# Kernel tuning notes

Measured on AMD Instinct MI355X. Metric: run time of the kernel, lower is better.

## Reference

```python
import jax, jax.numpy as jnp
import numpy as np

IN_FEATURES = 4096
OUT_FEATURES = 4096
NNZ = 1677722  # round(0.1 * 4096 * 4096)
N_TOKENS = 8192


def setup_inputs() -> dict:
    key = jax.random.key(0)
    k1, k2, k3, k4 = jax.random.split(key, 4)
    inputs = jax.random.normal(k1, (N_TOKENS, IN_FEATURES), dtype=jnp.float32)
    bound = 1.0 / IN_FEATURES ** 0.5
    weights = jax.random.uniform(k2, (NNZ,), minval=-bound, maxval=bound, dtype=jnp.float32)
    bias = jax.random.uniform(k3, (OUT_FEATURES,), minval=-bound, maxval=bound, dtype=jnp.float32)
    # COO indices: row (output) and col (input) indices, sampled like np.random.choice
    flat = jax.random.randint(k4, (NNZ,), 0, IN_FEATURES * OUT_FEATURES)
    row_ind = flat // IN_FEATURES
    col_ind = flat % IN_FEATURES
    indices = jnp.stack((row_ind, col_ind)).astype(jnp.int64)
    return {"inputs": inputs, "weights": weights, "bias": bias, "indices": indices}


def reference(inputs, weights, bias, indices):
    # Densify COO weight (duplicates are summed, matching torch coalesce/to_dense)
    dense_w = jnp.zeros((OUT_FEATURES, IN_FEATURES), dtype=weights.dtype)
    dense_w = dense_w.at[indices[0], indices[1]].add(weights)
    # output = (W @ x^T)^T + b  ==  x @ W^T + b
    out = jnp.einsum('ni,oi->no', inputs, dense_w) + bias
    return out
```

## Files before the change

### kernel.cpp

```cpp
#include <hip/hip_runtime.h>

#define M_TOK 8192
#define NF    4096
#define KF    4096
#define NHALF 128

typedef __attribute__((ext_vector_type(8))) short bf16x8;
typedef __attribute__((ext_vector_type(4))) float f32x4;
typedef __attribute__((ext_vector_type(2))) short s16x2;

__device__ __forceinline__ unsigned short f2bf(float f) {
    unsigned u = __builtin_bit_cast(unsigned, f);
    u += 0x7FFFu + ((u >> 16) & 1u);
    return (unsigned short)(u >> 16);
}

__device__ __forceinline__ float bf2f(unsigned short b) {
    unsigned u = ((unsigned)b) << 16;
    return __builtin_bit_cast(float, u);
}

__device__ __forceinline__ void load_lds16(const unsigned short* g, unsigned short* l) {
    __builtin_amdgcn_global_load_lds(
        (const __attribute__((address_space(1))) unsigned int*)g,
        (__attribute__((address_space(3))) unsigned int*)l,
        16, 0, 0);
}

__device__ __forceinline__ void block_bar() {
    asm volatile("" ::: "memory");
    __builtin_amdgcn_s_barrier();
    asm volatile("" ::: "memory");
}

#define VMCNT(n) asm volatile("s_waitcnt vmcnt(" #n ")" ::: "memory")

__global__ void prep_zero_convx(const float4* __restrict__ X, ushort4* __restrict__ Xb,
                                uint4* __restrict__ Wb, int nx4, int nwb) {
    int i = blockIdx.x * blockDim.x + threadIdx.x;
    if (i < nwb) Wb[i] = (uint4){0u, 0u, 0u, 0u};
    if (i < nx4) {
        float4 v = X[i];
        ushort4 o;
        o.x = f2bf(v.x); o.y = f2bf(v.y); o.z = f2bf(v.z); o.w = f2bf(v.w);
        Xb[i] = o;
    }
}

__global__ void scatter_bf16(const int* __restrict__ idx, const float* __restrict__ w,
                             unsigned short* __restrict__ Wb, int nnz) {
    int t = blockIdx.x * blockDim.x + threadIdx.x;
    if (t >= nnz) return;
    int r = idx[t];
    int c = idx[nnz + t];
    size_t elem = (size_t)r * KF + c;
#if __has_builtin(__builtin_amdgcn_global_atomic_fadd_v2bf16)
    unsigned short wb = f2bf(w[t]);
    s16x2 val;
    if (elem & 1) { val[0] = 0; val[1] = (short)wb; }
    else          { val[0] = (short)wb; val[1] = 0; }
    __builtin_amdgcn_global_atomic_fadd_v2bf16(
        (__attribute__((address_space(1))) s16x2*)(Wb + (elem & ~(size_t)1)), val);
#else
    unsigned* addr = (unsigned*)(Wb + (elem & ~(size_t)1));
    float wf = w[t];
    unsigned old = __hip_atomic_load(addr, __ATOMIC_RELAXED, __HIP_MEMORY_SCOPE_AGENT), assumed;
    do {
        assumed = old;
        unsigned short cur = (elem & 1) ? (unsigned short)(assumed >> 16)
                                        : (unsigned short)(assumed & 0xffffu);
        unsigned short nw = f2bf(bf2f(cur) + wf);
        unsigned newv = (elem & 1) ? ((assumed & 0x0000ffffu) | ((unsigned)nw << 16))
                                   : ((assumed & 0xffff0000u) | (unsigned)nw);
        old = atomicCAS(addr, assumed, newv);
    } while (old != assumed);
#endif
}

__global__ __launch_bounds__(512, 2) void gemm_bt_bias(
    const unsigned short* __restrict__ A,
    const unsigned short* __restrict__ B,
    const float* __restrict__ bias,
    float* __restrict__ C)
{
    __shared__ unsigned short lds_u[65536];
    char* const ldsb = (char*)lds_u;

    const int tid  = threadIdx.x;
    const int lane = tid & 63;
    const int wave = tid >> 6;
    const int wm   = wave >> 2;
    const int wn   = wave & 3;

    const int flat = blockIdx.y * 32 + blockIdx.x;
    const int xcd  = flat & 7;
    const int q    = flat >> 3;
    const int bm   = (xcd & 3) * 8 + (q & 7);
    const int bn   = (xcd >> 2) * 8 + (q >> 3);

    f32x4 acc[8][4] = {};

    const int gc   = (lane & 3) ^ ((lane >> 3) & 3);
    const int srow = wave * 16 + (lane >> 2);
    const unsigned short* gA   = A + (size_t)(bm * 256 + srow) * KF + gc * 8;
    const unsigned short* gB   = B + (size_t)(bn * 256 + srow) * KF + gc * 8;
    const unsigned short* gAHi = gA + (size_t)128 * KF;
    const unsigned short* gBHi = gB + (size_t)128 * KF;

    unsigned short* const sd = lds_u + wave * 512;

    const int fr    = lane & 15;
    const int quad  = lane >> 4;
    const int pos16 = (quad ^ ((fr >> 1) & 3)) << 4;
    const int rdA   = (wm * 128 + fr) * 64 + pos16;
    const int rdB   = 16384 + (wn * 64 + fr) * 64 + pos16;

#define STAGE_A(sb, ko) do { \
    load_lds16(gA   + (ko), sd + (((sb)        ) >> 1)); \
    load_lds16(gAHi + (ko), sd + (((sb) +  8192) >> 1)); \
} while (0)
#define STAGE_B(sb, ko) do { \
    load_lds16(gB   + (ko), sd + (((sb) + 16384) >> 1)); \
    load_lds16(gBHi + (ko), sd + (((sb) + 24576) >> 1)); \
} while (0)

#define RD_ALO(dst, sb) do { \
    _Pragma("unroll") \
    for (int _i = 0; _i < 4; ++_i) \
        dst[_i] = *(const bf16x8*)(ldsb + (sb) + rdA + _i * 1024); \
} while (0)

#define RD_AHI(dst, sb) do { \
    _Pragma("unroll") \
    for (int _i = 0; _i < 4; ++_i) \
        dst[_i] = *(const bf16x8*)(ldsb + (sb) + rdA + (4 + _i) * 1024); \
} while (0)

#define RD_B(dst, sb) do { \
    _Pragma("unroll") \
    for (int _j = 0; _j < 4; ++_j) \
        dst[_j] = *(const bf16x8*)(ldsb + (sb) + rdB + _j * 1024); \
} while (0)

#define MFMA16(i0, af, bfv) do { \
    _Pragma("unroll") \
    for (int _i = 0; _i < 4; ++_i) \
        _Pragma("unroll") \
        for (int _j = 0; _j < 4; ++_j) \
            acc[(i0) + _i][_j] = __builtin_amdgcn_mfma_f32_16x16x32_bf16(af[_i], bfv[_j], acc[(i0) + _i][_j], 0, 0, 0); \
} while (0)

    bf16x8 a_lo[4], a_hi[4], b1[4], b2[4];

#define HALF(G, BC, BN) do { \
    const int sb_  = ((G) & 3) << 15; \
    const int sbn_ = (((G) + 1) & 3) << 15; \
    const int sbs_ = (((G) + 3) & 3) << 15; \
    const int ko_  = ((G) + 3) * 32; \
    STAGE_A(sbs_, ko_); \
    STAGE_B(sbs_, ko_); \
    RD_AHI(a_hi, sb_); \
    RD_B(BN, sbn_); \
    __builtin_amdgcn_s_setprio(1); \
    MFMA16(0, a_lo, BC); \
    __builtin_amdgcn_s_setprio(0); \
    RD_ALO(a_lo, sbn_); \
    __builtin_amdgcn_s_setprio(1); \
    MFMA16(4, a_hi, BC); \
    __builtin_amdgcn_s_setprio(0); \
    VMCNT(4); \
    block_bar(); \
} while (0)

    STAGE_A(0, 0);       STAGE_B(0, 0);
    STAGE_A(32768, 32);  STAGE_B(32768, 32);
    STAGE_A(65536, 64);  STAGE_B(65536, 64);
    VMCNT(4);
    block_bar();
    RD_ALO(a_lo, 0);
    RD_B(b1, 0);

#pragma unroll 1
    for (int gp = 0; gp < 62; ++gp) {
        const int g = gp * 2;
        HALF(g,     b1, b2);
        HALF(g + 1, b2, b1);
    }
    HALF(124, b1, b2);

    {
        RD_AHI(a_hi, 32768);
        RD_B(b1, 65536);
        __builtin_amdgcn_s_setprio(1);
        MFMA16(0, a_lo, b2);
        __builtin_amdgcn_s_setprio(0);
        RD_ALO(a_lo, 65536);
        __builtin_amdgcn_s_setprio(1);
        MFMA16(4, a_hi, b2);
        __builtin_amdgcn_s_setprio(0);
        VMCNT(0);
        block_bar();
        RD_AHI(a_hi, 65536);
        RD_B(b2, 98304);
        MFMA16(0, a_lo, b1);
        RD_ALO(a_lo, 98304);
        MFMA16(4, a_hi, b1);
        RD_AHI(a_hi, 98304);
        MFMA16(0, a_lo, b2);
        MFMA16(4, a_hi, b2);
    }

#undef STAGE_A
#undef STAGE_B
#undef RD_ALO
#undef RD_AHI
#undef RD_B
#undef MFMA16
#undef HALF

    const int crow = bm * 256 + wm * 128;
    const int ccol = bn * 256 + wn * 64;
    const int r_l  = quad * 4;
#pragma unroll
    for (int j = 0; j < 4; ++j) {
        int col = ccol + j * 16 + fr;
        float bv = bias[col];
#pragma unroll
        for (int i = 0; i < 8; ++i) {
#pragma unroll
            for (int r = 0; r < 4; ++r)
                C[(size_t)(crow + i * 16 + r_l + r) * NF + col] = acc[i][j][r] + bv;
        }
    }
}

extern "C" void kernel_launch(void* const* d_in, const int* in_sizes, int n_in,
                              void* d_out, int out_size, void* d_ws, size_t ws_size,
                              hipStream_t stream) {
    const float* x    = (const float*)d_in[0];
    const float* w    = (const float*)d_in[1];
    const float* bias = (const float*)d_in[2];
    const int*   idx  = (const int*)d_in[3];
    float* out = (float*)d_out;
    const int nnz = in_sizes[1];

    unsigned short* Wb = (unsigned short*)d_ws;
    unsigned short* Xb = (unsigned short*)((char*)d_ws + (size_t)NF * KF * sizeof(unsigned short));

    const int nx4 = M_TOK * KF / 4;
    const int nwb = NF * KF * 2 / 16;

    prep_zero_convx<<<(nx4 + 255) / 256, 256, 0, stream>>>(
        (const float4*)x, (ushort4*)Xb, (uint4*)Wb, nx4, nwb);
    scatter_bf16<<<(nnz + 255) / 256, 256, 0, stream>>>(idx, w, Wb, nnz);
    gemm_bt_bias<<<dim3(32, 16), 512, 0, stream>>>(Xb, Wb, bias, out);
}
```

Measured before the change: 527.8 us.

## Hand-schedule LDS reads with inline asm and explicit lgkmcnt waits

Replaces compiler-generated LDS fragment loads with inline ds_read_b128 using immediate offsets, and unrolls the main loop by four so buffer slots are compile-time constants. Global pointers are now advanced incrementally. Explicit lgkmcnt waits and sched_barriers pin when MFMAs wait for LDS data, so reads overlap the preceding MFMA block. The intent is fewer address computations and finer-grained overlap of LDS reads with matrix math. The risk is that the manual waits are wrong, or that pinning the schedule blocks better compiler interleaving.

```diff
diff --git a/kernel.cpp b/kernel.cpp
--- a/kernel.cpp
+++ b/kernel.cpp
@@ -34,6 +34,10 @@
 }
 
 #define VMCNT(n) asm volatile("s_waitcnt vmcnt(" #n ")" ::: "memory")
+#define LGKM(n) do { \
+    asm volatile("s_waitcnt lgkmcnt(" #n ")" ::: "memory"); \
+    __builtin_amdgcn_sched_barrier(0); \
+} while (0)
 
 __global__ void prep_zero_convx(const float4* __restrict__ X, ushort4* __restrict__ Xb,
                                 uint4* __restrict__ Wb, int nx4, int nwb) {
@@ -84,7 +88,6 @@
     float* __restrict__ C)
 {
     __shared__ unsigned short lds_u[65536];
-    char* const ldsb = (char*)lds_u;
 
     const int tid  = threadIdx.x;
     const int lane = tid & 63;
@@ -115,32 +118,33 @@
     const int rdA   = (wm * 128 + fr) * 64 + pos16;
     const int rdB   = 16384 + (wn * 64 + fr) * 64 + pos16;
 
-#define STAGE_A(sb, ko) do { \
-    load_lds16(gA   + (ko), sd + (((sb)        ) >> 1)); \
-    load_lds16(gAHi + (ko), sd + (((sb) +  8192) >> 1)); \
-} while (0)
-#define STAGE_B(sb, ko) do { \
-    load_lds16(gB   + (ko), sd + (((sb) + 16384) >> 1)); \
-    load_lds16(gBHi + (ko), sd + (((sb) + 24576) >> 1)); \
-} while (0)
-
-#define RD_ALO(dst, sb) do { \
-    _Pragma("unroll") \
-    for (int _i = 0; _i < 4; ++_i) \
-        dst[_i] = *(const bf16x8*)(ldsb + (sb) + rdA + _i * 1024); \
-} while (0)
-
-#define RD_AHI(dst, sb) do { \
-    _Pragma("unroll") \
-    for (int _i = 0; _i < 4; ++_i) \
-        dst[_i] = *(const bf16x8*)(ldsb + (sb) + rdA + (4 + _i) * 1024); \
-} while (0)
-
-#define RD_B(dst, sb) do { \
-    _Pragma("unroll") \
-    for (int _j = 0; _j < 4; ++_j) \
-        dst[_j] = *(const bf16x8*)(ldsb + (sb) + rdB + _j * 1024); \
-} while (0)
+    const unsigned base3 =
+        (unsigned)(size_t)(__attribute__((address_space(3))) unsigned short*)lds_u;
+    const unsigned aA0 = base3 + (unsigned)rdA;
+    const unsigned aA1 = aA0 + 65536u;
+    const unsigned aB0 = base3 + (unsigned)rdB;
+    const unsigned aB1 = aB0 + 65536u;
+
+#define RDA(dst, S, I) \
+    asm volatile("ds_read_b128 %0, %1 offset:%2" \
+        : "=v"(dst) : "v"((S) >= 2 ? aA1 : aA0), "i"((((S) & 1) * 32768) + (I) * 1024))
+#define RDB(dst, S, J) \
+    asm volatile("ds_read_b128 %0, %1 offset:%2" \
+        : "=v"(dst) : "v"((S) >= 2 ? aB1 : aB0), "i"((((S) & 1) * 32768) + (J) * 1024))
+#define RDA4(dst, S, I0) do { \
+    RDA(dst[0], S, (I0) + 0); RDA(dst[1], S, (I0) + 1); \
+    RDA(dst[2], S, (I0) + 2); RDA(dst[3], S, (I0) + 3); } while (0)
+#define RDB4(dst, S) do { \
+    RDB(dst[0], S, 0); RDB(dst[1], S, 1); \
+    RDB(dst[2], S, 2); RDB(dst[3], S, 3); } while (0)
+
+#define STAGE_A(SB) do { \
+    load_lds16(gA,   sd + (((SB)         ) >> 1)); \
+    load_lds16(gAHi, sd + (((SB) +  8192) >> 1)); } while (0)
+#define STAGE_B(SB) do { \
+    load_lds16(gB,   sd + (((SB) + 16384) >> 1)); \
+    load_lds16(gBHi, sd + (((SB) + 24576) >> 1)); } while (0)
+#define ADV do { gA += 32; gB += 32; gAHi += 32; gBHi += 32; } while (0)
 
 #define MFMA16(i0, af, bfv) do { \
     _Pragma("unroll") \
@@ -152,19 +156,20 @@
 
     bf16x8 a_lo[4], a_hi[4], b1[4], b2[4];
 
-#define HALF(G, BC, BN) do { \
-    const int sb_  = ((G) & 3) << 15; \
-    const int sbn_ = (((G) + 1) & 3) << 15; \
-    const int sbs_ = (((G) + 3) & 3) << 15; \
-    const int ko_  = ((G) + 3) * 32; \
-    STAGE_A(sbs_, ko_); \
-    STAGE_B(sbs_, ko_); \
-    RD_AHI(a_hi, sb_); \
-    RD_B(BN, sbn_); \
+#define HALF(SLOT, BC, BN) do { \
+    STAGE_A((((SLOT) + 3) & 3) * 32768); \
+    STAGE_B((((SLOT) + 3) & 3) * 32768); \
+    ADV; \
+    RDA4(a_hi, (SLOT), 4); \
+    RDB4(BN, (((SLOT) + 1) & 3)); \
+    __builtin_amdgcn_sched_barrier(0); \
+    LGKM(8); \
     __builtin_amdgcn_s_setprio(1); \
     MFMA16(0, a_lo, BC); \
     __builtin_amdgcn_s_setprio(0); \
-    RD_ALO(a_lo, sbn_); \
+    RDA4(a_lo, (((SLOT) + 1) & 3), 0); \
+    __builtin_amdgcn_sched_barrier(0); \
+    LGKM(8); \
     __builtin_amdgcn_s_setprio(1); \
     MFMA16(4, a_hi, BC); \
     __builtin_amdgcn_s_setprio(0); \
@@ -172,49 +177,71 @@
     block_bar(); \
 } while (0)
 
-    STAGE_A(0, 0);       STAGE_B(0, 0);
-    STAGE_A(32768, 32);  STAGE_B(32768, 32);
-    STAGE_A(65536, 64);  STAGE_B(65536, 64);
+    STAGE_A(0);     STAGE_B(0);     ADV;
+    STAGE_A(32768); STAGE_B(32768); ADV;
+    STAGE_A(65536); STAGE_B(65536); ADV;
     VMCNT(4);
     block_bar();
-    RD_ALO(a_lo, 0);
-    RD_B(b1, 0);
+    RDA4(a_lo, 0, 0);
+    RDB4(b1, 0);
 
 #pragma unroll 1
-    for (int gp = 0; gp < 62; ++gp) {
-        const int g = gp * 2;
-        HALF(g,     b1, b2);
-        HALF(g + 1, b2, b1);
-    }
-    HALF(124, b1, b2);
+    for (int t = 0; t < 31; ++t) {
+        HALF(0, b1, b2);
+        HALF(1, b2, b1);
+        HALF(2, b1, b2);
+        HALF(3, b2, b1);
+    }
+    HALF(0, b1, b2);
 
     {
-        RD_AHI(a_hi, 32768);
-        RD_B(b1, 65536);
+        RDA4(a_hi, 1, 4);
+        RDB4(b1, 2);
+        __builtin_amdgcn_sched_barrier(0);
+        LGKM(8);
         __builtin_amdgcn_s_setprio(1);
         MFMA16(0, a_lo, b2);
         __builtin_amdgcn_s_setprio(0);
-        RD_ALO(a_lo, 65536);
+        RDA4(a_lo, 2, 0);
+        __builtin_amdgcn_sched_barrier(0);
+        LGKM(8);
         __builtin_amdgcn_s_setprio(1);
         MFMA16(4, a_hi, b2);
         __builtin_amdgcn_s_setprio(0);
         VMCNT(0);
         block_bar();
-        RD_AHI(a_hi, 65536);
-        RD_B(b2, 98304);
+        RDA4(a_hi, 2, 4);
+        __builtin_amdgcn_sched_barrier(0);
+        LGKM(4);
+        __builtin_amdgcn_s_setprio(1);
         MFMA16(0, a_lo, b1);
-        RD_ALO(a_lo, 98304);
+        __builtin_amdgcn_s_setprio(0);
+        RDB4(b2, 3);
+        RDA4(a_lo, 3, 0);
+        __builtin_amdgcn_sched_barrier(0);
+        LGKM(8);
+        __builtin_amdgcn_s_setprio(1);
         MFMA16(4, a_hi, b1);
-        RD_AHI(a_hi, 98304);
+        __builtin_amdgcn_s_setprio(0);
+        RDA4(a_hi, 3, 4);
+        __builtin_amdgcn_sched_barrier(0);
+        LGKM(4);
+        __builtin_amdgcn_s_setprio(1);
         MFMA16(0, a_lo, b2);
+        __builtin_amdgcn_s_setprio(0);
+        LGKM(0);
+        __builtin_amdgcn_s_setprio(1);
         MFMA16(4, a_hi, b2);
-    }
-
+        __builtin_amdgcn_s_setprio(0);
+    }
+
+#undef RDA
+#undef RDB
+#undef RDA4
+#undef RDB4
 #undef STAGE_A
 #undef STAGE_B
-#undef RD_ALO
-#undef RD_AHI
-#undef RD_B
+#undef ADV
 #undef MFMA16
 #undef HALF
 
```

Result: faster. 514.7 us (-2.5%).
